# Optimization experiments

Hardware: AMD Instinct MI355X
Metric: run time of the kernel (lower is better)

The kernel has to match this reference:

```python
import jax, jax.numpy as jnp
import numpy as np
from jax import lax

B, L, V, EMB = 256, 256, 14, 512
K = 16  # LSH bits (capped so 2**k fits int32)


def _conv2d(x, w, b):
    # x: [B,C,H,W], w: [O,I,3,3], padding=1 -> SAME
    y = lax.conv_general_dilated(x, w, (1, 1), ((1, 1), (1, 1)),
                                 dimension_numbers=("NCHW", "OIHW", "NCHW"))
    return y + b[None, :, None, None]


def _maxpool1d(x):  # [B,C,L] -> [B,C,L//2], kernel=stride=2
    b, c, l = x.shape
    return x.reshape(b, c, l // 2, 2).max(-1)


def _branch(tokens, emb, cw, cb, lw, lb):
    # Embedding -> pool over sequence -> Conv2d(3x3,pad1) on [C, L//2, 1] -> Linear
    e = emb[tokens]                     # [B,L,512]
    e = jnp.transpose(e, (0, 2, 1))     # [B,512,L]
    e = _maxpool1d(e)[..., None]        # [B,512,L//2,1]
    e = _conv2d(e, cw, cb)              # [B,256,L//2,1]
    return e.reshape(e.shape[0], -1) @ lw + lb


def _fog_of_war(enemy_out, rand_proj):
    # lsh_hash: random projection -> sign bits -> integer representation
    bits = (enemy_out @ rand_proj > 0).astype(jnp.int32)          # [B,K]
    pow2 = 2 ** jnp.arange(K - 1, -1, -1, dtype=jnp.int32)
    integer_repr = (bits * pow2).sum(axis=1)                      # [B] (computed as in original; loop doesn't read it)
    n = integer_repr.shape[0]
    # Greedy loop: remainder starts as arange(n); all counts are 1, so argmax
    # picks the first remaining index each iteration, which is then removed.
    def step(mask, _):
        idx = jnp.argmax(mask)  # first True = smallest remaining index
        return mask.at[idx].set(False), idx
    _, order = lax.scan(step, jnp.ones((n,), jnp.bool_), None, length=n)
    return order  # == arange(n), the original's deterministic result


def setup_inputs() -> dict:
    key = jax.random.key(0)
    ks = jax.random.split(key, 18)
    s = 0.02
    return {
        "x": jax.random.randint(ks[0], (B, L), 0, V, dtype=jnp.int32),
        "enemy_emb": jax.random.normal(ks[1], (V, EMB), jnp.float32) * s,
        "enemy_conv_w": jax.random.normal(ks[2], (256, 512, 3, 3), jnp.float32) * s,
        "enemy_conv_b": jax.random.normal(ks[3], (256,), jnp.float32) * s,
        "enemy_lin_w": jax.random.normal(ks[4], (256 * (L // 2), 128), jnp.float32) * s,
        "enemy_lin_b": jax.random.normal(ks[5], (128,), jnp.float32) * s,
        "rand_proj": jax.random.normal(ks[6], (128, K), jnp.float32),
        "manip_conv_w": jax.random.normal(ks[7], (64, 128, 3, 3), jnp.float32) * s,
        "manip_conv_b": jax.random.normal(ks[8], (64,), jnp.float32) * s,
        "manip_lin_w": jax.random.normal(ks[9], (64 * (L // 2), 256), jnp.float32) * s,
        "manip_lin_b": jax.random.normal(ks[10], (256,), jnp.float32) * s,
        "friend_emb": jax.random.normal(ks[11], (V, EMB), jnp.float32) * s,
        "friend_conv_w": jax.random.normal(ks[12], (256, 512, 3, 3), jnp.float32) * s,
        "friend_conv_b": jax.random.normal(ks[13], (256,), jnp.float32) * s,
        "friend_lin1_w": jax.random.normal(ks[14], (256 * (L // 2), 128), jnp.float32) * s,
        "friend_lin1_b": jax.random.normal(ks[15], (128,), jnp.float32) * s,
        "friend_lin2_w": jax.random.normal(ks[16], (128, V), jnp.float32) * s,
        "friend_lin2_b": jax.random.normal(ks[17], (V,), jnp.float32) * s,
    }


def reference(x, enemy_emb, enemy_conv_w, enemy_conv_b, enemy_lin_w, enemy_lin_b,
              rand_proj, manip_conv_w, manip_conv_b, manip_lin_w, manip_lin_b,
              friend_emb, friend_conv_w, friend_conv_b, friend_lin1_w, friend_lin1_b,
              friend_lin2_w, friend_lin2_b):
    # enemy branch
    enemy_out = jax.nn.softmax(
        _branch(x, enemy_emb, enemy_conv_w, enemy_conv_b, enemy_lin_w, enemy_lin_b), axis=1)  # [B,128]
    # fog_of_war: LSH hash + greedy set-cover loop -> index order
    perm = _fog_of_war(enemy_out, rand_proj)  # [B] int
    # probability manipulator: Conv2d(128,64) expects [B,128,L//2,1]
    m_in = jnp.broadcast_to(enemy_out[perm][:, :, None, None], (B, 128, L // 2, 1))
    m = jax.nn.relu(_conv2d(m_in, manip_conv_w, manip_conv_b))   # [B,64,L//2,1]
    m = m.reshape(B, -1) @ manip_lin_w + manip_lin_b             # [B,256]
    # friend branch consumes manipulator output as a token sequence (Embedding needs ints)
    tokens = (jnp.floor(jnp.abs(m) * 100.0) % V).astype(jnp.int32)  # [B,256]
    f = _branch(tokens, friend_emb, friend_conv_w, friend_conv_b, friend_lin1_w, friend_lin1_b)
    f = f @ friend_lin2_w + friend_lin2_b                        # [B,14]
    return jax.nn.softmax(f, axis=1)
```

## Files before the change

kernel.cpp:

```cpp
#include <hip/hip_runtime.h>
#include <hip/hip_bf16.h>
#include <math.h>

#define BB    256
#define LL    256
#define NV    14
#define EMBD  512
#define H2    128
#define OC    256
#define NP    196
#define JD    128
#define MO    64
#define MJ    256

#define PB_CWT    256
#define PB_MANIPW 96
#define PB_LINT   64

using s16x8 = __attribute__((ext_vector_type(8))) short;
using f32x4 = __attribute__((ext_vector_type(4))) float;

static __device__ __forceinline__ unsigned short f2bf_rne(float f) {
    unsigned int u = __float_as_uint(f);
    unsigned int r = (u + 0x7FFFu + ((u >> 16) & 1u)) >> 16;
    return (unsigned short)r;
}
static __device__ __forceinline__ float bf2f(unsigned short h) {
    return __uint_as_float(((unsigned int)h) << 16);
}

__global__ void k_prep(const float* __restrict__ cw_e, const float* __restrict__ cw_f,
                       const float* __restrict__ mcw, const float* __restrict__ mlw,
                       float* __restrict__ cwT, float* __restrict__ Wc,
                       float* __restrict__ Lint) {
    __shared__ float T[48][66];
    int bid = blockIdx.x;
    int t = threadIdx.x;
    if (bid < PB_CWT) {
        int cb = bid;
        int ic = cb & 31;
        int oc = (cb >> 5) & 3;
        int br = cb >> 7;
        int i0 = ic * 16, o0 = oc * 64;
        const float* cw = br ? cw_f : cw_e;
        int ol = t >> 2, part = t & 3;
        const float* src = cw + ((size_t)(o0 + ol) * EMBD + i0) * 9 + part * 36;
        #pragma unroll
        for (int ii = 0; ii < 4; ++ii)
            #pragma unroll
            for (int kh = 0; kh < 3; ++kh)
                T[kh * 16 + part * 4 + ii][ol] = src[ii * 9 + kh * 3 + 1];
        __syncthreads();
        int lane = t & 63, r0 = t >> 6;
        for (int rr = r0; rr < 48; rr += 4) {
            int kh = rr >> 4, il = rr & 15;
            cwT[(((size_t)(br * 3 + kh)) * EMBD + i0 + il) * OC + o0 + lane] = T[rr][lane];
        }
    } else if (bid < PB_CWT + PB_MANIPW) {
        int idx = (bid - PB_CWT) * 256 + t;
        int o = idx & 63;
        int i = (idx >> 6) & 127;
        int cls = idx >> 13;
        const float* base = mcw + ((size_t)(o * 128 + i) * 3) * 3 + 1;
        float v = 0.f;
        if (cls != 2) { v += base[3]; v += base[6]; }
        else          { v += base[0]; v += base[3]; }
        if (cls == 1)   v += base[0];
        Wc[idx] = v;
    } else {
        int o = bid - (PB_CWT + PB_MANIPW);
        float s = 0.f;
        for (int h = 1; h <= 126; h++)
            s += mlw[((size_t)(o * H2 + h)) * MJ + t];
        Lint[o * 256 + t] = s;
    }
}

__global__ __launch_bounds__(512) void k_contrib(
        const float* __restrict__ emb_e, const float* __restrict__ emb_f,
        const float* __restrict__ cwT,
        const float* __restrict__ cb_e, const float* __restrict__ cb_f,
        float* __restrict__ C) {
    int bid = blockIdx.x;
    int qg = bid % 49;
    int kh = (bid / 49) % 3;
    int br = bid / 147;
    int t = threadIdx.x;
    int o = t & 255, ih = t >> 8;
    const float* emb = br ? emb_f : emb_e;

    __shared__ float Pl[4][512];
    __shared__ float Rd[4][2][256];
    for (int idx = t; idx < 4 * 512; idx += 512) {
        int row = idx >> 9, col = idx & 511;
        int q = qg * 4 + row;
        int t1 = q / NV, t2 = q % NV;
        Pl[row][col] = fmaxf(emb[t1 * EMBD + col], emb[t2 * EMBD + col]);
    }
    __syncthreads();

    const float* w = cwT + ((size_t)(br * 3 + kh) * EMBD + ih * 256) * OC + o;
    float acc[4] = {0.f, 0.f, 0.f, 0.f};
    #pragma unroll 8
    for (int i = 0; i < 256; i++) {
        float wv = w[(size_t)i * OC];
        #pragma unroll
        for (int qq = 0; qq < 4; qq++) acc[qq] = fmaf(wv, Pl[qq][ih * 256 + i], acc[qq]);
    }
    #pragma unroll
    for (int qq = 0; qq < 4; qq++) Rd[qq][ih][o] = acc[qq];
    __syncthreads();
    if (t < 256) {
        float cbv = (kh == 1) ? (br ? cb_f[o] : cb_e[o]) : 0.f;
        #pragma unroll
        for (int qq = 0; qq < 4; qq++)
            C[(((size_t)br * NP + qg * 4 + qq) * 3 + kh) * OC + o] =
                Rd[qq][0][o] + Rd[qq][1][o] + cbv;
    }
}

template <int X3, int SK>
__global__ __launch_bounds__(512) void k_gemm(
        const int* __restrict__ tok, const float* __restrict__ C,
        const float* __restrict__ lw, float* __restrict__ partial) {
    __shared__ unsigned short Ah[2][64][SK + 4];
    __shared__ unsigned short Al[X3 ? 2 : 1][X3 ? 64 : 1][X3 ? SK + 4 : 1];
    __shared__ unsigned short Bh[2][128][SK + 4];
    __shared__ unsigned short Bl[X3 ? 2 : 1][X3 ? 128 : 1][X3 ? SK + 4 : 1];

    const int h  = blockIdx.x;
    const int B0 = blockIdx.y * 64;
    const int t  = threadIdx.x;
    constexpr int NST = 256 / SK;
    constexpr int KQ  = SK / 8;
    constexpr int KPT = SK / 16;

    const int am = t >> 3;
    const int kq = (t & 7) * KQ;
    const int* tb = tok + (size_t)(B0 + am) * LL;
    const int q1 = tb[2 * h] * NV + tb[2 * h + 1];
    const float* r1 = C + ((size_t)q1 * 3 + 1) * OC + kq;
    const float* r0 = nullptr;
    const float* r2 = nullptr;
    if (h > 0)      { int q0 = tb[2 * h - 2] * NV + tb[2 * h - 1]; r0 = C + ((size_t)q0 * 3 + 0) * OC + kq; }
    if (h < H2 - 1) { int q2 = tb[2 * h + 2] * NV + tb[2 * h + 3]; r2 = C + ((size_t)q2 * 3 + 2) * OC + kq; }

    const int j0b = (t & 31) * 4;
    const int k0  = (t >> 5) * KPT;
    const float* wsrc = lw + (((size_t)k0 * H2) + h) * JD + j0b;

    float4 ya[SK / 32], yb[SK / 32], yc[SK / 32], wv4[KPT];

    auto load = [&](int s) {
        #pragma unroll
        for (int p = 0; p < SK / 32; ++p) {
            ya[p] = *(const float4*)(r1 + s * SK + 4 * p);
            if (r0) yb[p] = *(const float4*)(r0 + s * SK + 4 * p);
            else    yb[p] = make_float4(0, 0, 0, 0);
            if (r2) yc[p] = *(const float4*)(r2 + s * SK + 4 * p);
            else    yc[p] = make_float4(0, 0, 0, 0);
        }
        #pragma unroll
        for (int kk = 0; kk < KPT; ++kk)
            wv4[kk] = *(const float4*)(wsrc + ((size_t)(s * SK) + kk) * (H2 * JD));
    };

    auto store = [&](int buf) {
        #pragma unroll
        for (int p = 0; p < SK / 32; ++p) {
            float y[4];
            y[0] = ya[p].x + yb[p].x + yc[p].x; y[1] = ya[p].y + yb[p].y + yc[p].y;
            y[2] = ya[p].z + yb[p].z + yc[p].z; y[3] = ya[p].w + yb[p].w + yc[p].w;
            unsigned short hi[4];
            #pragma unroll
            for (int e = 0; e < 4; ++e) hi[e] = f2bf_rne(y[e]);
            uint2 u;
            u.x = (unsigned)hi[0] | ((unsigned)hi[1] << 16);
            u.y = (unsigned)hi[2] | ((unsigned)hi[3] << 16);
            *(uint2*)&Ah[buf][am][kq + 4 * p] = u;
            if (X3) {
                unsigned short lo[4];
                #pragma unroll
                for (int e = 0; e < 4; ++e) lo[e] = f2bf_rne(y[e] - bf2f(hi[e]));
                uint2 v;
                v.x = (unsigned)lo[0] | ((unsigned)lo[1] << 16);
                v.y = (unsigned)lo[2] | ((unsigned)lo[3] << 16);
                *(uint2*)&Al[buf][am][kq + 4 * p] = v;
            }
        }
        #pragma unroll
        for (int jj = 0; jj < 4; ++jj) {
            unsigned short hb[KPT], lb[KPT];
            #pragma unroll
            for (int kk = 0; kk < KPT; ++kk) {
                float wf = ((const float*)&wv4[kk])[jj];
                hb[kk] = f2bf_rne(wf);
                if (X3) lb[kk] = f2bf_rne(wf - bf2f(hb[kk]));
            }
            if constexpr (KPT == 2) {
                *(unsigned*)&Bh[buf][j0b + jj][k0] = (unsigned)hb[0] | ((unsigned)hb[1] << 16);
                if (X3) *(unsigned*)&Bl[buf][j0b + jj][k0] = (unsigned)lb[0] | ((unsigned)lb[1] << 16);
            } else {
                uint2 u;
                u.x = (unsigned)hb[0] | ((unsigned)hb[1] << 16);
                u.y = (unsigned)hb[2] | ((unsigned)hb[3] << 16);
                *(uint2*)&Bh[buf][j0b + jj][k0] = u;
                if (X3) {
                    uint2 v;
                    v.x = (unsigned)lb[0] | ((unsigned)lb[1] << 16);
                    v.y = (unsigned)lb[2] | ((unsigned)lb[3] << 16);
                    *(uint2*)&Bl[buf][j0b + jj][k0] = v;
                }
            }
        }
    };

    const int lane = t & 63, wid = t >> 6;
    const int Wm = (wid >> 2) * 32;
    const int Wn = (wid & 3) * 32;
    const int fr = lane & 15;
    const int g8 = (lane >> 4) * 8;

    f32x4 acc[2][2] = {};

    auto rd8 = [&](const unsigned short* p) -> s16x8 {
        union { s16x8 v; uint2 u[2]; } tmp;
        tmp.u[0] = *(const uint2*)(p);
        tmp.u[1] = *(const uint2*)(p + 4);
        return tmp.v;
    };

    auto compute = [&](int buf) {
        #pragma unroll
        for (int kk0 = 0; kk0 < SK; kk0 += 32) {
            s16x8 a_h[2], b_h[2];
            #pragma unroll
            for (int mf = 0; mf < 2; ++mf) a_h[mf] = rd8(&Ah[buf][Wm + mf * 16 + fr][kk0 + g8]);
            #pragma unroll
            for (int nf = 0; nf < 2; ++nf) b_h[nf] = rd8(&Bh[buf][Wn + nf * 16 + fr][kk0 + g8]);
            #pragma unroll
            for (int mf = 0; mf < 2; ++mf)
                #pragma unroll
                for (int nf = 0; nf < 2; ++nf)
                    acc[mf][nf] = __builtin_amdgcn_mfma_f32_16x16x32_bf16(a_h[mf], b_h[nf], acc[mf][nf], 0, 0, 0);
            if (X3) {
                s16x8 a_l[2], b_l[2];
                #pragma unroll
                for (int mf = 0; mf < 2; ++mf) a_l[mf] = rd8(&Al[buf][Wm + mf * 16 + fr][kk0 + g8]);
                #pragma unroll
                for (int nf = 0; nf < 2; ++nf) b_l[nf] = rd8(&Bl[buf][Wn + nf * 16 + fr][kk0 + g8]);
                #pragma unroll
                for (int mf = 0; mf < 2; ++mf)
                    #pragma unroll
                    for (int nf = 0; nf < 2; ++nf) {
                        acc[mf][nf] = __builtin_amdgcn_mfma_f32_16x16x32_bf16(a_h[mf], b_l[nf], acc[mf][nf], 0, 0, 0);
                        acc[mf][nf] = __builtin_amdgcn_mfma_f32_16x16x32_bf16(a_l[mf], b_h[nf], acc[mf][nf], 0, 0, 0);
                    }
            }
        }
    };

    load(0);
    store(0);
    __syncthreads();
    for (int s = 0; s < NST; ++s) {
        if (s < NST - 1) load(s + 1);
        compute(s & 1);
        if (s < NST - 1) store((s + 1) & 1);
        __syncthreads();
    }

    float* pb = partial + (((size_t)(B0 + Wm)) * H2 + h) * JD + Wn;
    #pragma unroll
    for (int mf = 0; mf < 2; ++mf)
        #pragma unroll
        for (int nf = 0; nf < 2; ++nf)
            #pragma unroll
            for (int r = 0; r < 4; ++r) {
                int row = mf * 16 + (lane >> 4) * 4 + r;
                int col = nf * 16 + fr;
                pb[(size_t)row * H2 * JD + col] = acc[mf][nf][r];
            }
}

__global__ __launch_bounds__(256) void k_fuseE(
        const float* __restrict__ partial, const float* __restrict__ elb,
        const float* __restrict__ Wc, const float* __restrict__ mcb,
        const float* __restrict__ mlw, const float* __restrict__ Lint,
        const float* __restrict__ mlb, int* __restrict__ tokens) {
    int b = blockIdx.x, t = threadIdx.x;
    __shared__ float S[2][128];
    __shared__ float eo[128];
    __shared__ float m3[3][64];
    __shared__ float red[128];

    int j = t & 127, hh = t >> 7;
    float s = 0.f;
    const float* pbase = partial + (size_t)b * H2 * JD + j;
    for (int h = hh * 64; h < hh * 64 + 64; ++h)
        s += pbase[(size_t)h * JD];
    S[hh][j] = s;
    __syncthreads();
    if (t < 128) {
        float v = S[0][t] + S[1][t] + elb[t];
        S[0][t] = v;
        red[t] = v;
    }
    __syncthreads();
    for (int st = 64; st > 0; st >>= 1) {
        if (t < st) red[t] = fmaxf(red[t], red[t + st]);
        __syncthreads();
    }
    float mx = red[0];
    __syncthreads();
    if (t < 128) {
        float e = expf(S[0][t] - mx);
        eo[t] = e;
        red[t] = e;
    }
    __syncthreads();
    for (int st = 64; st > 0; st >>= 1) {
        if (t < st) red[t] += red[t + st];
        __syncthreads();
    }
    float inv = 1.f / red[0];
    __syncthreads();
    if (t < 128) eo[t] *= inv;
    __syncthreads();
    if (t < 192) {
        int cls = t >> 6, o = t & 63;
        float a = mcb[o];
        const float* wp = Wc + (size_t)cls * 128 * 64 + o;
        for (int i = 0; i < 128; ++i) a = fmaf(eo[i], wp[(size_t)i * 64], a);
        m3[cls][o] = fmaxf(a, 0.f);
    }
    __syncthreads();
    float a = mlb[t];
    for (int o = 0; o < MO; ++o) {
        a = fmaf(m3[0][o], mlw[((size_t)(o * H2 + 0)) * MJ + t], a);
        a = fmaf(m3[1][o], Lint[(size_t)o * MJ + t], a);
        a = fmaf(m3[2][o], mlw[((size_t)(o * H2 + 127)) * MJ + t], a);
    }
    tokens[(size_t)b * LL + t] = ((int)floorf(fabsf(a) * 100.f)) % NV;
}

__global__ __launch_bounds__(256) void k_fuseF(
        const float* __restrict__ partial, const float* __restrict__ flb1,
        const float* __restrict__ fl2, const float* __restrict__ fb2,
        float* __restrict__ outp) {
    int b = blockIdx.x, t = threadIdx.x;
    __shared__ float S[2][128];
    __shared__ float f1[128];
    __shared__ float sl[NV];
    int j = t & 127, hh = t >> 7;
    float s = 0.f;
    const float* pbase = partial + (size_t)b * H2 * JD + j;
    for (int h = hh * 64; h < hh * 64 + 64; ++h)
        s += pbase[(size_t)h * JD];
    S[hh][j] = s;
    __syncthreads();
    if (t < 128) f1[t] = S[0][t] + S[1][t] + flb1[t];
    __syncthreads();
    if (t < NV) {
        float a = fb2[t];
        for (int jj = 0; jj < 128; ++jj) a = fmaf(f1[jj], fl2[(size_t)jj * NV + t], a);
        sl[t] = a;
    }
    __syncthreads();
    if (t < NV) {
        float mx = -1e30f;
        for (int u = 0; u < NV; ++u) mx = fmaxf(mx, sl[u]);
        float ss = 0.f;
        for (int u = 0; u < NV; ++u) ss += expf(sl[u] - mx);
        outp[(size_t)b * NV + t] = expf(sl[t] - mx) / ss;
    }
}

extern "C" void kernel_launch(void* const* d_in, const int* in_sizes, int n_in,
                              void* d_out, int out_size, void* d_ws, size_t ws_size,
                              hipStream_t stream) {
    const int*   x    = (const int*)d_in[0];
    const float* eemb = (const float*)d_in[1];
    const float* ecw  = (const float*)d_in[2];
    const float* ecb  = (const float*)d_in[3];
    const float* elw  = (const float*)d_in[4];
    const float* elb  = (const float*)d_in[5];
    const float* mcw  = (const float*)d_in[7];
    const float* mcb  = (const float*)d_in[8];
    const float* mlw  = (const float*)d_in[9];
    const float* mlb  = (const float*)d_in[10];
    const float* femb = (const float*)d_in[11];
    const float* fcw  = (const float*)d_in[12];
    const float* fcb  = (const float*)d_in[13];
    const float* flw1 = (const float*)d_in[14];
    const float* flb1 = (const float*)d_in[15];
    const float* fl2  = (const float*)d_in[16];
    const float* fb2  = (const float*)d_in[17];
    float* outp = (float*)d_out;

    char* w = (char*)d_ws;
    size_t off = 0;
    auto alloc = [&](size_t bytes) {
        void* p = w + off;
        off = (off + bytes + 255) & ~(size_t)255;
        return p;
    };
    float* cwT    = (float*)alloc(2ull * 3 * EMBD * OC * 4);
    float* C      = (float*)alloc(2ull * NP * 3 * OC * 4);
    float* Wc     = (float*)alloc(3ull * 128 * 64 * 4);
    float* Lint   = (float*)alloc(64ull * MJ * 4);
    int*   tokens = (int*)alloc((size_t)BB * LL * 4);
    float* partial= (float*)alloc((size_t)BB * H2 * JD * 4);

    const float* C_e = C;
    const float* C_f = C + (size_t)NP * 3 * OC;

    k_prep<<<PB_CWT + PB_MANIPW + PB_LINT, 256, 0, stream>>>(
        ecw, fcw, mcw, mlw, cwT, Wc, Lint);
    k_contrib<<<2 * 3 * 49, 512, 0, stream>>>(eemb, femb, cwT, ecb, fcb, C);

    k_gemm<1, 32><<<dim3(H2, 4), 512, 0, stream>>>(x, C_e, elw, partial);
    k_fuseE<<<BB, 256, 0, stream>>>(partial, elb, Wc, mcb, mlw, Lint, mlb, tokens);

    k_gemm<0, 64><<<dim3(H2, 4), 512, 0, stream>>>(tokens, C_f, flw1, partial);
    k_fuseF<<<BB, 256, 0, stream>>>(partial, flb1, fl2, fb2, outp);
}
```

Measured before the change: 81.07 us.

## Add single-stage 128x128 tile GEMM kernel for friend branch linear layer

Replaces the generic pipelined k_gemm for the friend branch with a dedicated kernel that uses 128-row M tiles (grid halved in y), loads the full K=256 slice of A and B into shared memory at once, and runs the MFMA loop with a 4x2 fragment layout per wave. This removes the multi-stage double-buffer loop and halves the number of blocks re-reading the weight slice, which cuts redundant weight traffic. The cost is larger shared memory per block (about 135 KB) and fewer blocks (256), which can lower occupancy and latency hiding.

```diff
diff --git a/kernel.cpp b/kernel.cpp
--- a/kernel.cpp
+++ b/kernel.cpp
@@ -273,6 +273,109 @@
     float* pb = partial + (((size_t)(B0 + Wm)) * H2 + h) * JD + Wn;
     #pragma unroll
     for (int mf = 0; mf < 2; ++mf)
+        #pragma unroll
+        for (int nf = 0; nf < 2; ++nf)
+            #pragma unroll
+            for (int r = 0; r < 4; ++r) {
+                int row = mf * 16 + (lane >> 4) * 4 + r;
+                int col = nf * 16 + fr;
+                pb[(size_t)row * H2 * JD + col] = acc[mf][nf][r];
+            }
+}
+
+__global__ __launch_bounds__(512) void k_gemmF1(
+        const int* __restrict__ tok, const float* __restrict__ C,
+        const float* __restrict__ lw, float* __restrict__ partial) {
+    __shared__ unsigned short Ab[128][264];
+    __shared__ unsigned short Bb[128][264];
+
+    const int h  = blockIdx.x;
+    const int B0 = blockIdx.y * 128;
+    const int t  = threadIdx.x;
+
+    const int am = t >> 2;
+    const int kq = (t & 3) * 64;
+    const int* tb = tok + (size_t)(B0 + am) * LL;
+    const int q1 = tb[2 * h] * NV + tb[2 * h + 1];
+    const float* r1 = C + ((size_t)q1 * 3 + 1) * OC + kq;
+    const float* r0 = nullptr;
+    const float* r2 = nullptr;
+    if (h > 0)      { int q0 = tb[2 * h - 2] * NV + tb[2 * h - 1]; r0 = C + ((size_t)q0 * 3 + 0) * OC + kq; }
+    if (h < H2 - 1) { int q2 = tb[2 * h + 2] * NV + tb[2 * h + 3]; r2 = C + ((size_t)q2 * 3 + 2) * OC + kq; }
+
+    #pragma unroll
+    for (int p = 0; p < 16; ++p) {
+        float4 a = *(const float4*)(r1 + 4 * p);
+        float4 b = r0 ? *(const float4*)(r0 + 4 * p) : make_float4(0, 0, 0, 0);
+        float4 c = r2 ? *(const float4*)(r2 + 4 * p) : make_float4(0, 0, 0, 0);
+        unsigned short h0 = f2bf_rne(a.x + b.x + c.x);
+        unsigned short h1 = f2bf_rne(a.y + b.y + c.y);
+        unsigned short h2 = f2bf_rne(a.z + b.z + c.z);
+        unsigned short h3 = f2bf_rne(a.w + b.w + c.w);
+        uint2 u;
+        u.x = (unsigned)h0 | ((unsigned)h1 << 16);
+        u.y = (unsigned)h2 | ((unsigned)h3 << 16);
+        *(uint2*)&Ab[am][kq + 4 * p] = u;
+    }
+
+    const int j0b = (t & 31) * 4;
+    const int k0  = (t >> 5) * 16;
+    const float* wsrc = lw + ((size_t)k0 * H2 + h) * JD + j0b;
+    #pragma unroll
+    for (int cchunk = 0; cchunk < 2; ++cchunk) {
+        unsigned short hb[4][8];
+        #pragma unroll
+        for (int kk = 0; kk < 8; ++kk) {
+            float4 v = *(const float4*)(wsrc + ((size_t)(cchunk * 8 + kk)) * (H2 * JD));
+            hb[0][kk] = f2bf_rne(v.x);
+            hb[1][kk] = f2bf_rne(v.y);
+            hb[2][kk] = f2bf_rne(v.z);
+            hb[3][kk] = f2bf_rne(v.w);
+        }
+        #pragma unroll
+        for (int jj = 0; jj < 4; ++jj) {
+            uint2 u0, u1;
+            u0.x = (unsigned)hb[jj][0] | ((unsigned)hb[jj][1] << 16);
+            u0.y = (unsigned)hb[jj][2] | ((unsigned)hb[jj][3] << 16);
+            u1.x = (unsigned)hb[jj][4] | ((unsigned)hb[jj][5] << 16);
+            u1.y = (unsigned)hb[jj][6] | ((unsigned)hb[jj][7] << 16);
+            *(uint2*)&Bb[j0b + jj][k0 + cchunk * 8]     = u0;
+            *(uint2*)&Bb[j0b + jj][k0 + cchunk * 8 + 4] = u1;
+        }
+    }
+    __syncthreads();
+
+    const int lane = t & 63, wid = t >> 6;
+    const int Wm = (wid >> 2) * 64;
+    const int Wn = (wid & 3) * 32;
+    const int fr = lane & 15;
+    const int g8 = (lane >> 4) * 8;
+
+    f32x4 acc[4][2] = {};
+
+    auto rd8 = [&](const unsigned short* p) -> s16x8 {
+        union { s16x8 v; uint2 u[2]; } tmp;
+        tmp.u[0] = *(const uint2*)(p);
+        tmp.u[1] = *(const uint2*)(p + 4);
+        return tmp.v;
+    };
+
+    for (int ks = 0; ks < 8; ++ks) {
+        s16x8 a_h[4], b_h[2];
+        #pragma unroll
+        for (int mf = 0; mf < 4; ++mf) a_h[mf] = rd8(&Ab[Wm + mf * 16 + fr][ks * 32 + g8]);
+        #pragma unroll
+        for (int nf = 0; nf < 2; ++nf) b_h[nf] = rd8(&Bb[Wn + nf * 16 + fr][ks * 32 + g8]);
+        #pragma unroll
+        for (int mf = 0; mf < 4; ++mf)
+            #pragma unroll
+            for (int nf = 0; nf < 2; ++nf)
+                acc[mf][nf] = __builtin_amdgcn_mfma_f32_16x16x32_bf16(a_h[mf], b_h[nf], acc[mf][nf], 0, 0, 0);
+    }
+
+    float* pb = partial + (((size_t)(B0 + Wm)) * H2 + h) * JD + Wn;
+    #pragma unroll
+    for (int mf = 0; mf < 4; ++mf)
         #pragma unroll
         for (int nf = 0; nf < 2; ++nf)
             #pragma unroll
@@ -422,6 +525,6 @@
     k_gemm<1, 32><<<dim3(H2, 4), 512, 0, stream>>>(x, C_e, elw, partial);
     k_fuseE<<<BB, 256, 0, stream>>>(partial, elb, Wc, mcb, mlw, Lint, mlb, tokens);
 
-    k_gemm<0, 64><<<dim3(H2, 4), 512, 0, stream>>>(tokens, C_f, flw1, partial);
+    k_gemmF1<<<dim3(H2, 2), 512, 0, stream>>>(tokens, C_f, flw1, partial);
     k_fuseF<<<BB, 256, 0, stream>>>(partial, flb1, fl2, fb2, outp);
 }
```

Result: slower. 89.01 us (+9.8%).

## Move manip weight prep into contrib kernel and widen fuse kernels to 512 threads

Applied to the files above, without the earlier changes.

Moves the Wc and Lint precomputation blocks out of k_prep and into k_contrib as extra blocks, so k_prep only transposes the conv weights and becomes shorter on the critical path. Those extra blocks now run alongside the contrib blocks, and each uses 512 threads. k_fuseE and k_fuseF are launched with 512 threads: the partial-sum reduction splits into four slices, and the manipulator linear layer splits its output-channel loop across two halves that are combined through shared memory. This adds more parallelism per batch row, at the cost of an extra sync and more shared memory.

```diff
diff --git a/kernel.cpp b/kernel.cpp
--- a/kernel.cpp
+++ b/kernel.cpp
@@ -13,9 +13,9 @@
 #define MO    64
 #define MJ    256
 
-#define PB_CWT    256
-#define PB_MANIPW 96
-#define PB_LINT   64
+#define CB_MAIN   294
+#define CB_MANIPW 48
+#define CB_LINT   32
 
 using s16x8 = __attribute__((ext_vector_type(8))) short;
 using f32x4 = __attribute__((ext_vector_type(4))) float;
@@ -30,34 +30,75 @@
 }
 
 __global__ void k_prep(const float* __restrict__ cw_e, const float* __restrict__ cw_f,
-                       const float* __restrict__ mcw, const float* __restrict__ mlw,
-                       float* __restrict__ cwT, float* __restrict__ Wc,
-                       float* __restrict__ Lint) {
+                       float* __restrict__ cwT) {
     __shared__ float T[48][66];
     int bid = blockIdx.x;
     int t = threadIdx.x;
-    if (bid < PB_CWT) {
-        int cb = bid;
-        int ic = cb & 31;
-        int oc = (cb >> 5) & 3;
-        int br = cb >> 7;
-        int i0 = ic * 16, o0 = oc * 64;
-        const float* cw = br ? cw_f : cw_e;
-        int ol = t >> 2, part = t & 3;
-        const float* src = cw + ((size_t)(o0 + ol) * EMBD + i0) * 9 + part * 36;
-        #pragma unroll
-        for (int ii = 0; ii < 4; ++ii)
-            #pragma unroll
-            for (int kh = 0; kh < 3; ++kh)
-                T[kh * 16 + part * 4 + ii][ol] = src[ii * 9 + kh * 3 + 1];
+    int ic = bid & 31;
+    int oc = (bid >> 5) & 3;
+    int br = bid >> 7;
+    int i0 = ic * 16, o0 = oc * 64;
+    const float* cw = br ? cw_f : cw_e;
+    int ol = t >> 2, part = t & 3;
+    const float* src = cw + ((size_t)(o0 + ol) * EMBD + i0) * 9 + part * 36;
+    #pragma unroll
+    for (int ii = 0; ii < 4; ++ii)
+        #pragma unroll
+        for (int kh = 0; kh < 3; ++kh)
+            T[kh * 16 + part * 4 + ii][ol] = src[ii * 9 + kh * 3 + 1];
+    __syncthreads();
+    int lane = t & 63, r0 = t >> 6;
+    for (int rr = r0; rr < 48; rr += 4) {
+        int kh = rr >> 4, il = rr & 15;
+        cwT[(((size_t)(br * 3 + kh)) * EMBD + i0 + il) * OC + o0 + lane] = T[rr][lane];
+    }
+}
+
+__global__ __launch_bounds__(512) void k_contrib(
+        const float* __restrict__ emb_e, const float* __restrict__ emb_f,
+        const float* __restrict__ cwT,
+        const float* __restrict__ cb_e, const float* __restrict__ cb_f,
+        const float* __restrict__ mcw, const float* __restrict__ mlw,
+        float* __restrict__ C, float* __restrict__ Wc, float* __restrict__ Lint) {
+    int bid = blockIdx.x;
+    int t = threadIdx.x;
+    if (bid < CB_MAIN) {
+        int qg = bid % 49;
+        int kh = (bid / 49) % 3;
+        int br = bid / 147;
+        int o = t & 255, ih = t >> 8;
+        const float* emb = br ? emb_f : emb_e;
+
+        __shared__ float Pl[4][512];
+        __shared__ float Rd[4][2][256];
+        for (int idx = t; idx < 4 * 512; idx += 512) {
+            int row = idx >> 9, col = idx & 511;
+            int q = qg * 4 + row;
+            int t1 = q / NV, t2 = q % NV;
+            Pl[row][col] = fmaxf(emb[t1 * EMBD + col], emb[t2 * EMBD + col]);
+        }
         __syncthreads();
-        int lane = t & 63, r0 = t >> 6;
-        for (int rr = r0; rr < 48; rr += 4) {
-            int kh = rr >> 4, il = rr & 15;
-            cwT[(((size_t)(br * 3 + kh)) * EMBD + i0 + il) * OC + o0 + lane] = T[rr][lane];
-        }
-    } else if (bid < PB_CWT + PB_MANIPW) {
-        int idx = (bid - PB_CWT) * 256 + t;
+
+        const float* w = cwT + ((size_t)(br * 3 + kh) * EMBD + ih * 256) * OC + o;
+        float acc[4] = {0.f, 0.f, 0.f, 0.f};
+        #pragma unroll 8
+        for (int i = 0; i < 256; i++) {
+            float wv = w[(size_t)i * OC];
+            #pragma unroll
+            for (int qq = 0; qq < 4; qq++) acc[qq] = fmaf(wv, Pl[qq][ih * 256 + i], acc[qq]);
+        }
+        #pragma unroll
+        for (int qq = 0; qq < 4; qq++) Rd[qq][ih][o] = acc[qq];
+        __syncthreads();
+        if (t < 256) {
+            float cbv = (kh == 1) ? (br ? cb_f[o] : cb_e[o]) : 0.f;
+            #pragma unroll
+            for (int qq = 0; qq < 4; qq++)
+                C[(((size_t)br * NP + qg * 4 + qq) * 3 + kh) * OC + o] =
+                    Rd[qq][0][o] + Rd[qq][1][o] + cbv;
+        }
+    } else if (bid < CB_MAIN + CB_MANIPW) {
+        int idx = (bid - CB_MAIN) * 512 + t;
         int o = idx & 63;
         int i = (idx >> 6) & 127;
         int cls = idx >> 13;
@@ -68,54 +109,13 @@
         if (cls == 1)   v += base[0];
         Wc[idx] = v;
     } else {
-        int o = bid - (PB_CWT + PB_MANIPW);
+        int lb = bid - (CB_MAIN + CB_MANIPW);
+        int o = lb * 2 + (t >> 8);
+        int j = t & 255;
         float s = 0.f;
         for (int h = 1; h <= 126; h++)
-            s += mlw[((size_t)(o * H2 + h)) * MJ + t];
-        Lint[o * 256 + t] = s;
-    }
-}
-
-__global__ __launch_bounds__(512) void k_contrib(
-        const float* __restrict__ emb_e, const float* __restrict__ emb_f,
-        const float* __restrict__ cwT,
-        const float* __restrict__ cb_e, const float* __restrict__ cb_f,
-        float* __restrict__ C) {
-    int bid = blockIdx.x;
-    int qg = bid % 49;
-    int kh = (bid / 49) % 3;
-    int br = bid / 147;
-    int t = threadIdx.x;
-    int o = t & 255, ih = t >> 8;
-    const float* emb = br ? emb_f : emb_e;
-
-    __shared__ float Pl[4][512];
-    __shared__ float Rd[4][2][256];
-    for (int idx = t; idx < 4 * 512; idx += 512) {
-        int row = idx >> 9, col = idx & 511;
-        int q = qg * 4 + row;
-        int t1 = q / NV, t2 = q % NV;
-        Pl[row][col] = fmaxf(emb[t1 * EMBD + col], emb[t2 * EMBD + col]);
-    }
-    __syncthreads();
-
-    const float* w = cwT + ((size_t)(br * 3 + kh) * EMBD + ih * 256) * OC + o;
-    float acc[4] = {0.f, 0.f, 0.f, 0.f};
-    #pragma unroll 8
-    for (int i = 0; i < 256; i++) {
-        float wv = w[(size_t)i * OC];
-        #pragma unroll
-        for (int qq = 0; qq < 4; qq++) acc[qq] = fmaf(wv, Pl[qq][ih * 256 + i], acc[qq]);
-    }
-    #pragma unroll
-    for (int qq = 0; qq < 4; qq++) Rd[qq][ih][o] = acc[qq];
-    __syncthreads();
-    if (t < 256) {
-        float cbv = (kh == 1) ? (br ? cb_f[o] : cb_e[o]) : 0.f;
-        #pragma unroll
-        for (int qq = 0; qq < 4; qq++)
-            C[(((size_t)br * NP + qg * 4 + qq) * 3 + kh) * OC + o] =
-                Rd[qq][0][o] + Rd[qq][1][o] + cbv;
+            s += mlw[((size_t)(o * H2 + h)) * MJ + j];
+        Lint[o * 256 + j] = s;
     }
 }
 
@@ -283,26 +283,27 @@
             }
 }
 
-__global__ __launch_bounds__(256) void k_fuseE(
+__global__ __launch_bounds__(512) void k_fuseE(
         const float* __restrict__ partial, const float* __restrict__ elb,
         const float* __restrict__ Wc, const float* __restrict__ mcb,
         const float* __restrict__ mlw, const float* __restrict__ Lint,
         const float* __restrict__ mlb, int* __restrict__ tokens) {
     int b = blockIdx.x, t = threadIdx.x;
-    __shared__ float S[2][128];
+    __shared__ float S[4][128];
     __shared__ float eo[128];
     __shared__ float m3[3][64];
     __shared__ float red[128];
+    __shared__ float mt[2][256];
 
     int j = t & 127, hh = t >> 7;
     float s = 0.f;
     const float* pbase = partial + (size_t)b * H2 * JD + j;
-    for (int h = hh * 64; h < hh * 64 + 64; ++h)
+    for (int h = hh * 32; h < hh * 32 + 32; ++h)
         s += pbase[(size_t)h * JD];
     S[hh][j] = s;
     __syncthreads();
     if (t < 128) {
-        float v = S[0][t] + S[1][t] + elb[t];
+        float v = (S[0][t] + S[1][t]) + (S[2][t] + S[3][t]) + elb[t];
         S[0][t] = v;
         red[t] = v;
     }
@@ -335,31 +336,39 @@
         m3[cls][o] = fmaxf(a, 0.f);
     }
     __syncthreads();
-    float a = mlb[t];
-    for (int o = 0; o < MO; ++o) {
-        a = fmaf(m3[0][o], mlw[((size_t)(o * H2 + 0)) * MJ + t], a);
-        a = fmaf(m3[1][o], Lint[(size_t)o * MJ + t], a);
-        a = fmaf(m3[2][o], mlw[((size_t)(o * H2 + 127)) * MJ + t], a);
-    }
-    tokens[(size_t)b * LL + t] = ((int)floorf(fabsf(a) * 100.f)) % NV;
-}
-
-__global__ __launch_bounds__(256) void k_fuseF(
+    {
+        int ihh = t >> 8, jj = t & 255;
+        float a = ihh ? 0.f : mlb[jj];
+        for (int o = ihh * 32; o < ihh * 32 + 32; ++o) {
+            a = fmaf(m3[0][o], mlw[((size_t)(o * H2 + 0)) * MJ + jj], a);
+            a = fmaf(m3[1][o], Lint[(size_t)o * MJ + jj], a);
+            a = fmaf(m3[2][o], mlw[((size_t)(o * H2 + 127)) * MJ + jj], a);
+        }
+        mt[ihh][jj] = a;
+    }
+    __syncthreads();
+    if (t < 256) {
+        float a = mt[0][t] + mt[1][t];
+        tokens[(size_t)b * LL + t] = ((int)floorf(fabsf(a) * 100.f)) % NV;
+    }
+}
+
+__global__ __launch_bounds__(512) void k_fuseF(
         const float* __restrict__ partial, const float* __restrict__ flb1,
         const float* __restrict__ fl2, const float* __restrict__ fb2,
         float* __restrict__ outp) {
     int b = blockIdx.x, t = threadIdx.x;
-    __shared__ float S[2][128];
+    __shared__ float S[4][128];
     __shared__ float f1[128];
     __shared__ float sl[NV];
     int j = t & 127, hh = t >> 7;
     float s = 0.f;
     const float* pbase = partial + (size_t)b * H2 * JD + j;
-    for (int h = hh * 64; h < hh * 64 + 64; ++h)
+    for (int h = hh * 32; h < hh * 32 + 32; ++h)
         s += pbase[(size_t)h * JD];
     S[hh][j] = s;
     __syncthreads();
-    if (t < 128) f1[t] = S[0][t] + S[1][t] + flb1[t];
+    if (t < 128) f1[t] = (S[0][t] + S[1][t]) + (S[2][t] + S[3][t]) + flb1[t];
     __syncthreads();
     if (t < NV) {
         float a = fb2[t];
@@ -415,13 +424,13 @@
     const float* C_e = C;
     const float* C_f = C + (size_t)NP * 3 * OC;
 
-    k_prep<<<PB_CWT + PB_MANIPW + PB_LINT, 256, 0, stream>>>(
-        ecw, fcw, mcw, mlw, cwT, Wc, Lint);
-    k_contrib<<<2 * 3 * 49, 512, 0, stream>>>(eemb, femb, cwT, ecb, fcb, C);
+    k_prep<<<256, 256, 0, stream>>>(ecw, fcw, cwT);
+    k_contrib<<<CB_MAIN + CB_MANIPW + CB_LINT, 512, 0, stream>>>(
+        eemb, femb, cwT, ecb, fcb, mcw, mlw, C, Wc, Lint);
 
     k_gemm<1, 32><<<dim3(H2, 4), 512, 0, stream>>>(x, C_e, elw, partial);
-    k_fuseE<<<BB, 256, 0, stream>>>(partial, elb, Wc, mcb, mlw, Lint, mlb, tokens);
+    k_fuseE<<<BB, 512, 0, stream>>>(partial, elb, Wc, mcb, mlw, Lint, mlb, tokens);
 
     k_gemm<0, 64><<<dim3(H2, 4), 512, 0, stream>>>(tokens, C_f, flw1, partial);
-    k_fuseF<<<BB, 256, 0, stream>>>(partial, flb1, fl2, fb2, outp);
-}
+    k_fuseF<<<BB, 512, 0, stream>>>(partial, flb1, fl2, fb2, outp);
+}
```

New measurement: 74.42 us, median of 2. 8.2% less time.
